# Performance work log

Hardware: AMD Instinct MI355X
Metric: run time of the kernel (lower is better)

## Reference

```python
import jax, jax.numpy as jnp
import numpy as np

# Dims from GlobalFractalRouterConfig defaults
B, D, FP, H, NF, A = 65536, 512, 64, 256, 4, 32


def _norm(x):
    # F.normalize(dim=-1) with eps=1e-12
    return x / jnp.clip(jnp.linalg.norm(x, axis=-1, keepdims=True), 1e-12)


def setup_inputs() -> dict:
    key = jax.random.key(0)
    ks = jax.random.split(key, 12)
    s = 0.02
    return {
        "features": jax.random.normal(ks[0], (B, D), jnp.float32),
        "source_fingerprint": jax.random.normal(ks[1], (FP,), jnp.float32),
        "target_fingerprint": jax.random.normal(ks[2], (FP,), jnp.float32),
        # field_generators: NF stacked (Linear(D+FP,H) -> GELU -> Linear(H,1))
        "Wf1": jax.random.normal(ks[3], (NF, D + FP, H), jnp.float32) * s,
        "bf1": jnp.zeros((NF, H), jnp.float32),
        "Wf2": jax.random.normal(ks[4], (NF, H), jnp.float32) * s,
        "bf2": jnp.zeros((NF,), jnp.float32),
        # compat_proj: Linear(2*FP, NF)
        "Wc": jax.random.normal(ks[5], (2 * FP, NF), jnp.float32) * s,
        "bc": jnp.zeros((NF,), jnp.float32),
        # gate_net: Linear(2*NF+FP, H) -> GELU -> Linear(H, D) -> Sigmoid
        "Wg1": jax.random.normal(ks[6], (2 * NF + FP, H), jnp.float32) * s,
        "bg1": jnp.zeros((H,), jnp.float32),
        "Wg2": jax.random.normal(ks[7], (H, D), jnp.float32) * s,
        "bg2": jnp.zeros((D,), jnp.float32),
        # AnchorBank
        "E": jax.random.normal(ks[8], (A, D), jnp.float32) * s,  # anchor_embeddings
        "Wfp": jax.random.normal(ks[9], (D, D), jnp.float32) * s,  # feature_proj
        "bfp": jnp.zeros((D,), jnp.float32),
        "Wfq": jax.random.normal(ks[10], (FP, D), jnp.float32) * s,  # fingerprint_proj
        "bfq": jnp.zeros((D,), jnp.float32),
    }


def _potential(feats, fp_vec, Wf1, bf1, Wf2, bf2):
    # AdjacentGate.compute_potential, all fields vectorized
    b = feats.shape[0]
    comb = jnp.concatenate(
        [feats, jnp.broadcast_to(fp_vec, (b, fp_vec.shape[0]))], axis=-1
    )  # [B, D+FP]
    h = jax.nn.gelu(jnp.einsum('bi,fih->bfh', comb, Wf1) + bf1, approximate=False)
    return jnp.einsum('bfh,fh->bf', h, Wf2) + bf2  # [B, NF]


def reference(features, source_fingerprint, target_fingerprint,
              Wf1, bf1, Wf2, bf2, Wc, bc, Wg1, bg1, Wg2, bg2,
              E, Wfp, bfp, Wfq, bfq):
    b = features.shape[0]
    # --- AdjacentGate ---
    p_src = _potential(features, source_fingerprint, Wf1, bf1, Wf2, bf2)
    p_tgt = _potential(features, target_fingerprint, Wf1, bf1, Wf2, bf2)
    gradient = p_tgt - p_src  # [B, NF]
    fp_comb = jnp.concatenate([source_fingerprint, target_fingerprint])  # [2*FP]
    compat = jnp.tanh(fp_comb @ Wc + bc)  # [NF]
    gate_in = jnp.concatenate(
        [gradient,
         jnp.broadcast_to(compat, (b, compat.shape[0])),
         jnp.broadcast_to(source_fingerprint, (b, source_fingerprint.shape[0]))],
        axis=-1)  # [B, 2*NF+FP]
    gate = jax.nn.sigmoid(
        jax.nn.gelu(gate_in @ Wg1 + bg1, approximate=False) @ Wg2 + bg2)  # [B, D]
    gated = features * gate
    # --- AnchorBank ---
    feat_proj = _norm(gated @ Wfp + bfp)  # [B, D]
    anchors_norm = _norm(E)  # [A, D]
    aff = feat_proj @ anchors_norm.T  # [B, A]
    fp_proj = source_fingerprint @ Wfq + bfq  # [D]
    aff = aff + 0.3 * (anchors_norm @ fp_proj)
    aff = jax.nn.softmax(aff, axis=-1)
    anchor_features = aff @ E  # [B, D]
    return gated + anchor_features
```

## Files before the change

### kernel.cpp

```cpp
#include <hip/hip_runtime.h>
#include <hip/hip_bf16.h>

typedef unsigned short u16;
typedef __attribute__((ext_vector_type(8))) __bf16 bf16x8;
typedef __attribute__((ext_vector_type(8))) short  s16x8;
typedef __attribute__((ext_vector_type(4))) short  s16x4;
typedef __attribute__((ext_vector_type(4))) float  f32x4;

#define NB 65536
#define OFF_GRAD   0u
#define OFF_SUMSQ  1048576u
#define OFF_CONSTS 1310720u
#define OFF_WF1T   1327104u
#define OFF_WG2T   2375680u
#define OFF_WFPT   2637824u
#define OFF_ET     3162112u
#define OFF_AFF    3194880u
#define OFF_GATED  7389184u
#define WS_NEEDED  74498048u
#define CI_SRC   0
#define CI_TGT   1024
#define CI_C0    2048
#define CI_INVE  2304
#define CI_ABIAS 2336

__device__ inline float bf2f(u16 u) { union { unsigned int i; float f; } v; v.i = ((unsigned int)u) << 16; return v.f; }
__device__ inline u16 f2bf(float f) { union { float f; unsigned int i; } v; v.f = f; return (u16)((v.i + 0x7fffu + ((v.i >> 16) & 1u)) >> 16); }
__device__ inline float gelu(float x) {
  float z = 1.5957691216f * x * (1.0f + 0.044715f * x * x);
  return x * __builtin_amdgcn_rcpf(1.0f + __expf(-z));
}
__device__ inline float sigm(float x) { return __builtin_amdgcn_rcpf(1.0f + __expf(-x)); }

typedef __attribute__((address_space(3))) unsigned int as3_u32;
typedef __attribute__((address_space(1))) unsigned int as1_u32;
__device__ __forceinline__ void gload16(const u16* g, u16* l) {
  __builtin_amdgcn_global_load_lds((const as1_u32*)g, (as3_u32*)l, 16, 0, 0);
}

__global__ __launch_bounds__(256) void k_cvt(const float* __restrict__ feat, u16* __restrict__ featbf) {
  int idx = (blockIdx.x << 8) + threadIdx.x;
  const float4* src = (const float4*)feat + (idx << 1);
  float4 v0 = src[0], v1 = src[1];
  s16x8 o;
  o[0] = (short)f2bf(v0.x); o[1] = (short)f2bf(v0.y);
  o[2] = (short)f2bf(v0.z); o[3] = (short)f2bf(v0.w);
  o[4] = (short)f2bf(v1.x); o[5] = (short)f2bf(v1.y);
  o[6] = (short)f2bf(v1.z); o[7] = (short)f2bf(v1.w);
  *(s16x8*)(featbf + (idx << 3)) = o;
}

__global__ __launch_bounds__(256) void k_pre(
    const float* __restrict__ sfp, const float* __restrict__ tfp,
    const float* __restrict__ wf1, const float* __restrict__ bf1,
    const float* __restrict__ wc,  const float* __restrict__ bc,
    const float* __restrict__ wg1, const float* __restrict__ bg1,
    const float* __restrict__ wfq, const float* __restrict__ bfq,
    const float* __restrict__ E,   float* __restrict__ consts)
{
  __shared__ float s_s[64], s_t[64], s_c[4], s_fp[512];
  const int t = threadIdx.x;
  const int b = blockIdx.x;
  if (t < 64) { s_s[t] = sfp[t]; s_t[t] = tfp[t]; }
  __syncthreads();
  if (b < 8) {
    if (t < 128) {
      int n = b * 128 + t;
      int f = n >> 8, h = n & 255;
      float as = bf1[f * 256 + h];
      float at = as;
      const float* col = wf1 + f * 147456 + 512 * 256 + h;
      #pragma unroll 8
// ... 37 lines not shown
  }
}

__global__ __launch_bounds__(256) void k_transpose(
    const float* __restrict__ wf1, const float* __restrict__ wg2,
    const float* __restrict__ wfp, const float* __restrict__ E,
    u16* __restrict__ ws16)
{
  int tile = blockIdx.x;
  const float* src; u16* dst; int K, N, tl;
  if (tile < 512)      { int f = tile >> 7; tl = tile & 127; src = wf1 + f * 147456; dst = ws16 + (OFF_WF1T >> 1) + f * 131072; K = 512; N = 256; }
  else if (tile < 640) { tl = tile - 512; src = wg2; dst = ws16 + (OFF_WG2T >> 1); K = 256; N = 512; }
  else if (tile < 896) { tl = tile - 640; src = wfp; dst = ws16 + (OFF_WFPT >> 1); K = 512; N = 512; }
  else                 { tl = tile - 896; src = E;   dst = ws16 + (OFF_ET   >> 1); K = 32;  N = 512; }
  int ntn = N >> 5;
  int r0 = (tl / ntn) << 5, c0 = (tl % ntn) << 5;
  __shared__ float T[32][33];
  const int t = threadIdx.x;
  {
    int r = t >> 3, c4 = (t & 7) << 2;
    float4 v = *(const float4*)(src + (r0 + r) * N + c0 + c4);
    T[r][c4] = v.x; T[r][c4 + 1] = v.y; T[r][c4 + 2] = v.z; T[r][c4 + 3] = v.w;
  }
  __syncthreads();
  {
    int c = t >> 3, r4 = (t & 7) << 2;
    s16x4 v;
    v[0] = (short)f2bf(T[r4 + 0][c]); v[1] = (short)f2bf(T[r4 + 1][c]);
    v[2] = (short)f2bf(T[r4 + 2][c]); v[3] = (short)f2bf(T[r4 + 3][c]);
    *(s16x4*)(dst + (c0 + c) * K + r0 + r4) = v;
  }
}

__global__ __launch_bounds__(256, 2) void k_potential(
    const u16* __restrict__ featbf, const u16* __restrict__ wf1t,
    const float* __restrict__ wf2,  const float* __restrict__ consts,
    float* __restrict__ grad)
{
  __shared__ u16 U[36864];
  const int wg = blockIdx.x;
  const int s  = ((wg & 7) << 8) + (wg >> 3);
  const int f  = s & 3;
  const int col0 = f << 8;
  const int row0 = (s >> 2) << 7;
  const int t = threadIdx.x;
  const int w = t >> 6, lane = t & 63, lr = lane & 15, lq = lane >> 4;
  const int gr  = lane >> 2;
  const int gcs = ((lane & 3) ^ ((lane >> 3) & 3)) << 3;
  const int ca  = (lq ^ ((lr >> 1) & 3)) << 3;

  f32x4 acc[2][16];
  #pragma unroll
  for (int i = 0; i < 2; ++i)
    #pragma unroll
    for (int j = 0; j < 16; ++j) { f32x4 z = {0.f, 0.f, 0.f, 0.f}; acc[i][j] = z; }

#define STAGE_P(bi, k0) { u16* bas = U + (bi) * 12288; \
    _Pragma("unroll") for (int j = 0; j < 2; ++j) { int rb = (j << 6) + (w << 4); \
      gload16(featbf + (row0 + rb + gr) * 512 + (k0) + gcs, bas + rb * 32); } \
    _Pragma("unroll") for (int j = 0; j < 4; ++j) { int rb = (j << 6) + (w << 4); \
      gload16(wf1t + (col0 + rb + gr) * 512 + (k0) + gcs, bas + 4096 + rb * 32); } }

#define COMP_P(bi) { const u16* bas = U + (bi) * 12288; bf16x8 a[2]; \
    _Pragma("unroll") for (int rt = 0; rt < 2; ++rt) \
      a[rt] = *(const bf16x8*)&bas[((w << 5) + (rt << 4) + lr) * 32 + ca]; \
    _Pragma("unroll") for (int ct = 0; ct < 16; ++ct) { \
      bf16x8 bb = *(const bf16x8*)&bas[4096 + ((ct << 4) + lr) * 32 + ca]; \
      acc[0][ct] = __builtin_amdgcn_mfma_f32_16x16x32_bf16(a[0], bb, acc[0][ct], 0, 0, 0); \
      acc[1][ct] = __builtin_amdgcn_mfma_f32_16x16x32_bf16(a[1], bb, acc[1][ct], 0, 0, 0); } }

  STAGE_P(0, 0);
  STAGE_P(1, 32);
  #pragma unroll
  for (int tt = 0; tt < 16; ++tt) {
    if (tt < 15) asm volatile("s_waitcnt vmcnt(6)\n\ts_barrier" ::: "memory");
    else         asm volatile("s_waitcnt vmcnt(0)\n\ts_barrier" ::: "memory");
    if (tt < 14) STAGE_P((tt + 2) % 3, (tt + 2) * 32);
    COMP_P(tt % 3);
  }
#undef STAGE_P
#undef COMP_P
  float part[2][4] = {{0, 0, 0, 0}, {0, 0, 0, 0}};
  #pragma unroll
  for (int ct = 0; ct < 16; ++ct) {
    int n = col0 + (ct << 4) + lr;
    float so = consts[CI_SRC + n];
    float to = consts[CI_TGT + n];
    float w2 = wf2[n];
    #pragma unroll
    for (int rt = 0; rt < 2; ++rt)
      #pragma unroll
      for (int j = 0; j < 4; ++j) {
        float c = acc[rt][ct][j];
        part[rt][j] += (gelu(c + to) - gelu(c + so)) * w2;
      }
  }
  #pragma unroll
  for (int m = 1; m <= 8; m <<= 1)
    #pragma unroll
    for (int rt = 0; rt < 2; ++rt)
      #pragma unroll
      for (int j = 0; j < 4; ++j)
        part[rt][j] += __shfl_xor(part[rt][j], m, 64);
  if (lr == 0) {
    #pragma unroll
    for (int rt = 0; rt < 2; ++rt)
      #pragma unroll
      for (int j = 0; j < 4; ++j) {
        int r = row0 + (w << 5) + (rt << 4) + (lq << 2) + j;
        grad[r * 4 + f] = part[rt][j];
      }
  }
}

__global__ __launch_bounds__(256, 2) void k_gate(
    const u16* __restrict__ featbf, const float* __restrict__ grad,
    const float* __restrict__ wg1,  const u16* __restrict__ wg2t,
    const float* __restrict__ bg2,  const float* __restrict__ consts,
    u16* __restrict__ gated)
{
  __shared__ u16 Hl[32768];
  __shared__ u16 Bl[2][128][32];
  const int wg = blockIdx.x;
  const int s  = ((wg & 7) << 8) + (wg >> 3);
  const int col0 = (s & 3) << 7;
  const int row0 = (s >> 2) << 7;
  const int t = threadIdx.x;
  const int w = t >> 6, lane = t & 63, lr = lane & 15, lq = lane >> 4;
  const int gr  = lane >> 2;
  const int gcs = ((lane & 3) ^ ((lane >> 3) & 3)) << 3;
  const int ca  = (lq ^ ((lr >> 1) & 3)) << 3;

#define STAGE_G(buf, k0) { \
    _Pragma("unroll") for (int j = 0; j < 2; ++j) { int rb = (j << 6) + (w << 4); \
      gload16(wg2t + (col0 + rb + gr) * 256 + (k0) + gcs, &Bl[buf][rb][0]); } }

  STAGE_G(0, 0);

  {
    float wv[4], c0v = consts[CI_C0 + t];
    const int tc = t >> 3, tw = t & 7;
    #pragma unroll
    for (int f = 0; f < 4; ++f) wv[f] = wg1[f * 256 + t];
    for (int i = 0; i < 128; ++i) {
// ... 28 lines not shown
    COMP_G(1, k0 + 32);
    __syncthreads();
  }
#undef STAGE_G
#undef COMP_G
  u16* Gl = Hl;
  #pragma unroll
  for (int ct = 0; ct < 8; ++ct) {
    int n = col0 + (ct << 4) + lr;
    float bv = bg2[n];
    #pragma unroll
    for (int rt = 0; rt < 2; ++rt)
      #pragma unroll
      for (int j = 0; j < 4; ++j) {
        int r = (w << 5) + (rt << 4) + (lq << 2) + j;
        Gl[r * 136 + (ct << 4) + lr] = f2bf(sigm(acc[rt][ct][j] + bv));
      }
  }
  __syncthreads();
  #pragma unroll
  for (int it = 0; it < 8; ++it) {
    int s2 = (it << 8) + t;
    int r = s2 >> 4, c8 = (s2 & 15) << 3;
    s16x8 f8 = *(const s16x8*)(featbf + (row0 + r) * 512 + col0 + c8);
    s16x8 g8 = *(const s16x8*)(Gl + r * 136 + c8);
    s16x8 o;
    #pragma unroll
    for (int j = 0; j < 8; ++j)
      o[j] = (short)f2bf(bf2f((u16)f8[j]) * bf2f((u16)g8[j]));
    *(s16x8*)(gated + (row0 + r) * 512 + col0 + c8) = o;
  }
}

__global__ __launch_bounds__(256, 2) void k_proj(
    const u16* __restrict__ gated, const u16* __restrict__ wfpt,
    const float* __restrict__ bfp, const float* __restrict__ E,
    float* __restrict__ aff32, float* __restrict__ sumsq)
{
  __shared__ u16 U[36864];
  const int wg = blockIdx.x;
  const int s  = ((wg & 7) << 7) + (wg >> 3);
  const int col0 = (s & 1) << 8;
  const int row0 = (s >> 1) << 7;
  const int t = threadIdx.x;
  const int w = t >> 6, lane = t & 63, lr = lane & 15, lq = lane >> 4;
  const int gr  = lane >> 2;
  const int gcs = ((lane & 3) ^ ((lane >> 3) & 3)) << 3;
  const int ca  = (lq ^ ((lr >> 1) & 3)) << 3;

  f32x4 acc[2][16];
  #pragma unroll
  for (int i = 0; i < 2; ++i)
    #pragma unroll
    for (int j = 0; j < 16; ++j) { f32x4 z = {0.f, 0.f, 0.f, 0.f}; acc[i][j] = z; }

#define STAGE_J(bi, k0) { u16* bas = U + (bi) * 12288; \
    _Pragma("unroll") for (int j = 0; j < 2; ++j) { int rb = (j << 6) + (w << 4); \
      gload16(gated + (row0 + rb + gr) * 512 + (k0) + gcs, bas + rb * 32); } \
    _Pragma("unroll") for (int j = 0; j < 4; ++j) { int rb = (j << 6) + (w << 4); \
      gload16(wfpt + (col0 + rb + gr) * 512 + (k0) + gcs, bas + 4096 + rb * 32); } }

#define COMP_J(bi) { const u16* bas = U + (bi) * 12288; bf16x8 a[2]; \
    _Pragma("unroll") for (int rt = 0; rt < 2; ++rt) \
      a[rt] = *(const bf16x8*)&bas[((w << 5) + (rt << 4) + lr) * 32 + ca]; \
    _Pragma("unroll") for (int ct = 0; ct < 16; ++ct) { \
      bf16x8 bb = *(const bf16x8*)&bas[4096 + ((ct << 4) + lr) * 32 + ca]; \
      acc[0][ct] = __builtin_amdgcn_mfma_f32_16x16x32_bf16(a[0], bb, acc[0][ct], 0, 0, 0); \
      acc[1][ct] = __builtin_amdgcn_mfma_f32_16x16x32_bf16(a[1], bb, acc[1][ct], 0, 0, 0); } }

  STAGE_J(0, 0);
  STAGE_J(1, 32);
  #pragma unroll
  for (int tt = 0; tt < 16; ++tt) {
    if (tt < 15) asm volatile("s_waitcnt vmcnt(6)\n\ts_barrier" ::: "memory");
    else         asm volatile("s_waitcnt vmcnt(0)\n\ts_barrier" ::: "memory");
    if (tt < 14) STAGE_J((tt + 2) % 3, (tt + 2) * 32);
    COMP_J(tt % 3);
  }
#undef STAGE_J
#undef COMP_J
  float part[2][4] = {{0, 0, 0, 0}, {0, 0, 0, 0}};
  #pragma unroll
  for (int ct = 0; ct < 16; ++ct) {
    float bv = bfp[col0 + (ct << 4) + lr];
    #pragma unroll
    for (int rt = 0; rt < 2; ++rt)
      #pragma unroll
      for (int j = 0; j < 4; ++j) {
        acc[rt][ct][j] += bv;
        part[rt][j] += acc[rt][ct][j] * acc[rt][ct][j];
      }
  }
  #pragma unroll
  for (int m = 1; m <= 8; m <<= 1)
    #pragma unroll
    for (int rt = 0; rt < 2; ++rt)
      #pragma unroll
      for (int j = 0; j < 4; ++j)
        part[rt][j] += __shfl_xor(part[rt][j], m, 64);
  if (lr == 0) {
    #pragma unroll
    for (int rt = 0; rt < 2; ++rt)
      #pragma unroll
      for (int j = 0; j < 4; ++j)
        atomicAdd(&sumsq[row0 + (w << 5) + (rt << 4) + (lq << 2) + j], part[rt][j]);
  }
  __syncthreads();
  {
    int a = t >> 3, cb = (t & 7) << 5;
    const float* ep = E + a * 512 + col0 + cb;
    u16* dp = U + 17408 + a * 264 + cb;
    #pragma unroll
    for (int i = 0; i < 8; ++i) {
      float4 v = *(const float4*)(ep + (i << 2));
      s16x4 b;
      b[0] = (short)f2bf(v.x); b[1] = (short)f2bf(v.y);
      b[2] = (short)f2bf(v.z); b[3] = (short)f2bf(v.w);
      *(s16x4*)(dp + (i << 2)) = b;
    }
  }
  f32x4 acc2[2][2];
  #pragma unroll
  for (int i = 0; i < 2; ++i)
    #pragma unroll
    for (int j = 0; j < 2; ++j) { f32x4 z = {0.f, 0.f, 0.f, 0.f}; acc2[i][j] = z; }
  #pragma unroll
  for (int half = 0; half < 2; ++half) {
    if (half) __syncthreads();
    #pragma unroll
    for (int ct = 0; ct < 8; ++ct)
      #pragma unroll
      for (int rt = 0; rt < 2; ++rt)
        #pragma unroll
        for (int j = 0; j < 4; ++j) {
          int r = (w << 5) + (rt << 4) + (lq << 2) + j;
          U[r * 136 + (ct << 4) + lr] = f2bf(acc[rt][(half << 3) + ct][j]);
        }
    __syncthreads();
    #pragma unroll
    for (int ks = 0; ks < 4; ++ks) {
      bf16x8 a0 = *(const bf16x8*)&U[((w << 5) + lr) * 136 + (ks << 5) + (lq << 3)];
      bf16x8 a1 = *(const bf16x8*)&U[((w << 5) + 16 + lr) * 136 + (ks << 5) + (lq << 3)];
      bf16x8 b0 = *(const bf16x8*)&U[17408 + lr * 264 + (half << 7) + (ks << 5) + (lq << 3)];
      bf16x8 b1 = *(const bf16x8*)&U[17408 + (16 + lr) * 264 + (half << 7) + (ks << 5) + (lq << 3)];
      acc2[0][0] = __builtin_amdgcn_mfma_f32_16x16x32_bf16(a0, b0, acc2[0][0], 0, 0, 0);
      acc2[0][1] = __builtin_amdgcn_mfma_f32_16x16x32_bf16(a0, b1, acc2[0][1], 0, 0, 0);
      acc2[1][0] = __builtin_amdgcn_mfma_f32_16x16x32_bf16(a1, b0, acc2[1][0], 0, 0, 0);
      acc2[1][1] = __builtin_amdgcn_mfma_f32_16x16x32_bf16(a1, b1, acc2[1][1], 0, 0, 0);
    }
  }
  #pragma unroll
  for (int rt = 0; rt < 2; ++rt)
    #pragma unroll
    for (int c2 = 0; c2 < 2; ++c2)
      #pragma unroll
      for (int j = 0; j < 4; ++j) {
        int r = row0 + (w << 5) + (rt << 4) + (lq << 2) + j;
        int a = (c2 << 4) + lr;
        atomicAdd(&aff32[(r << 5) + a], acc2[rt][c2][j]);
      }
}

__global__ __launch_bounds__(256) void k_softmax(
    const float* __restrict__ aff32, const float* __restrict__ sumsq,
    const float* __restrict__ consts, u16* __restrict__ aff)
{
  const int t = threadIdx.x;
  const int lane = t & 63, wv = t >> 6;
  const int a = lane & 31, rh = lane >> 5;
  float ive = consts[CI_INVE + a], ab = consts[CI_ABIAS + a];
  #pragma unroll
  for (int it = 0; it < 4; ++it) {
    int r = (blockIdx.x << 5) + (wv << 3) + (it << 1) + rh;
    float invy = 1.0f / fmaxf(sqrtf(sumsq[r]), 1e-12f);
    float v = aff32[(r << 5) + a] * ive * invy + ab;
    float mx = v;
    #pragma unroll
    for (int m = 1; m <= 16; m <<= 1) mx = fmaxf(mx, __shfl_xor(mx, m, 64));
    float e = __expf(v - mx);
    float sm = e;
    #pragma unroll
    for (int m = 1; m <= 16; m <<= 1) sm += __shfl_xor(sm, m, 64);
    aff[(r << 5) + a] = f2bf(e * (1.0f / sm));
  }
}

__global__ __launch_bounds__(256, 2) void k_out(
    const u16* __restrict__ gated, const u16* __restrict__ aff,
    const u16* __restrict__ et, float* __restrict__ out)
{
  __shared__ u16 ETl[512][40];
  __shared__ u16 Afl[64][40];
  __shared__ u16 Ol[64][520];
// ... 51 lines not shown
  const float* feat = (const float*)d_in[0];
  const float* sfp  = (const float*)d_in[1];
  const float* tfp  = (const float*)d_in[2];
  const float* wf1  = (const float*)d_in[3];
  const float* bf1  = (const float*)d_in[4];
  const float* wf2  = (const float*)d_in[5];
  const float* wc   = (const float*)d_in[7];
  const float* bc   = (const float*)d_in[8];
  const float* wg1  = (const float*)d_in[9];
  const float* bg1  = (const float*)d_in[10];
  const float* wg2  = (const float*)d_in[11];
  const float* bg2  = (const float*)d_in[12];
  const float* E    = (const float*)d_in[13];
  const float* wfp  = (const float*)d_in[14];
  const float* bfp  = (const float*)d_in[15];
  const float* wfq  = (const float*)d_in[16];
  const float* bfq  = (const float*)d_in[17];

  char* ws = (char*)d_ws;
  float* grad   = (float*)(ws + OFF_GRAD);
  float* sumsq  = (float*)(ws + OFF_SUMSQ);
  float* consts = (float*)(ws + OFF_CONSTS);
  u16* ws16  = (u16*)ws;
  u16* wf1t  = (u16*)(ws + OFF_WF1T);
  u16* wg2t  = (u16*)(ws + OFF_WG2T);
  u16* wfpt  = (u16*)(ws + OFF_WFPT);
  u16* et    = (u16*)(ws + OFF_ET);
  u16* aff   = (u16*)(ws + OFF_AFF);
  u16* gated = (u16*)(ws + OFF_GATED);
  float* aff32 = (float*)d_out;
  u16* featbf  = (u16*)d_out + 33554432;
  float* out = (float*)d_out;

  hipMemsetAsync(ws + OFF_SUMSQ, 0, 262144, stream);
  hipMemsetAsync(d_out, 0, 8388608, stream);
  k_cvt<<<dim3(16384), dim3(256), 0, stream>>>(feat, featbf);
  k_pre<<<dim3(10), dim3(256), 0, stream>>>(sfp, tfp, wf1, bf1, wc, bc, wg1, bg1, wfq, bfq, E, consts);
  k_transpose<<<dim3(912), dim3(256), 0, stream>>>(wf1, wg2, wfp, E, ws16);
  k_potential<<<dim3(2048), dim3(256), 0, stream>>>(featbf, wf1t, wf2, consts, grad);
  k_gate<<<dim3(2048), dim3(256), 0, stream>>>(featbf, grad, wg1, wg2t, bg2, consts, gated);
  k_proj<<<dim3(1024), dim3(256), 0, stream>>>(gated, wfpt, bfp, E, aff32, sumsq);
  k_softmax<<<dim3(2048), dim3(256), 0, stream>>>(aff32, sumsq, consts, aff);
  k_out<<<dim3(1024), dim3(256), 0, stream>>>(gated, aff, et, out);
}
```

Measured before the change: 608.2 us.

## Retile potential and proj GEMMs to 128x128 blocks with 2x2 warp layout

Both k_potential and k_proj drop their 128x256 per-block tiles, where each warp owned 32 rows by all columns, in favour of 128x128 tiles with a 2x2 arrangement of 64x64 warp tiles. They also replace the triple-buffered vmcnt pipeline with a simpler double buffer and raise occupancy to 3 blocks per CU. Because each block now covers only half a field's hidden columns, gradient partials go to grad through atomicAdd, so grad is zeroed by the widened memset. The intent is better register and LDS reuse per MFMA and more resident waves. The cost is twice as many blocks, more atomics, and a possibly weaker load pipeline.

```diff
diff --git a/kernel.cpp b/kernel.cpp
--- a/kernel.cpp
+++ b/kernel.cpp
@@ -141,63 +141,68 @@
   }
 }
 
-__global__ __launch_bounds__(256, 2) void k_potential(
+__global__ __launch_bounds__(256, 3) void k_potential(
     const u16* __restrict__ featbf, const u16* __restrict__ wf1t,
     const float* __restrict__ wf2,  const float* __restrict__ consts,
     float* __restrict__ grad)
 {
-  __shared__ u16 U[36864];
+  __shared__ u16 Al[2][128][32];
+  __shared__ u16 Bl[2][128][32];
   const int wg = blockIdx.x;
-  const int s  = ((wg & 7) << 8) + (wg >> 3);
-  const int f  = s & 3;
-  const int col0 = f << 8;
-  const int row0 = (s >> 2) << 7;
+  const int s  = ((wg & 7) << 9) + (wg >> 3);
+  const int col0 = (s & 7) << 7;
+  const int f    = col0 >> 8;
+  const int row0 = (s >> 3) << 7;
   const int t = threadIdx.x;
   const int w = t >> 6, lane = t & 63, lr = lane & 15, lq = lane >> 4;
   const int gr  = lane >> 2;
   const int gcs = ((lane & 3) ^ ((lane >> 3) & 3)) << 3;
   const int ca  = (lq ^ ((lr >> 1) & 3)) << 3;
-
-  f32x4 acc[2][16];
-  #pragma unroll
-  for (int i = 0; i < 2; ++i)
-    #pragma unroll
-    for (int j = 0; j < 16; ++j) { f32x4 z = {0.f, 0.f, 0.f, 0.f}; acc[i][j] = z; }
-
-#define STAGE_P(bi, k0) { u16* bas = U + (bi) * 12288; \
+  const int wr = (w >> 1) << 6;
+  const int wc = (w & 1) << 6;
+
+  f32x4 acc[4][4];
+  #pragma unroll
+  for (int i = 0; i < 4; ++i)
+    #pragma unroll
+    for (int j = 0; j < 4; ++j) { f32x4 z = {0.f, 0.f, 0.f, 0.f}; acc[i][j] = z; }
+
+#define STAGE_P(buf, k0) { \
     _Pragma("unroll") for (int j = 0; j < 2; ++j) { int rb = (j << 6) + (w << 4); \
-      gload16(featbf + (row0 + rb + gr) * 512 + (k0) + gcs, bas + rb * 32); } \
-    _Pragma("unroll") for (int j = 0; j < 4; ++j) { int rb = (j << 6) + (w << 4); \
-      gload16(wf1t + (col0 + rb + gr) * 512 + (k0) + gcs, bas + 4096 + rb * 32); } }
-
-#define COMP_P(bi) { const u16* bas = U + (bi) * 12288; bf16x8 a[2]; \
-    _Pragma("unroll") for (int rt = 0; rt < 2; ++rt) \
-      a[rt] = *(const bf16x8*)&bas[((w << 5) + (rt << 4) + lr) * 32 + ca]; \
-    _Pragma("unroll") for (int ct = 0; ct < 16; ++ct) { \
-      bf16x8 bb = *(const bf16x8*)&bas[4096 + ((ct << 4) + lr) * 32 + ca]; \
-      acc[0][ct] = __builtin_amdgcn_mfma_f32_16x16x32_bf16(a[0], bb, acc[0][ct], 0, 0, 0); \
-      acc[1][ct] = __builtin_amdgcn_mfma_f32_16x16x32_bf16(a[1], bb, acc[1][ct], 0, 0, 0); } }
+      gload16(featbf + (row0 + rb + gr) * 512 + (k0) + gcs, &Al[buf][rb][0]); \
+      gload16(wf1t   + (col0 + rb + gr) * 512 + (k0) + gcs, &Bl[buf][rb][0]); } }
+
+#define COMP_P(buf) { bf16x8 a[4], b[4]; \
+    _Pragma("unroll") for (int rt = 0; rt < 4; ++rt) \
+      a[rt] = *(const bf16x8*)&Al[buf][wr + (rt << 4) + lr][ca]; \
+    _Pragma("unroll") for (int ct = 0; ct < 4; ++ct) \
+      b[ct] = *(const bf16x8*)&Bl[buf][wc + (ct << 4) + lr][ca]; \
+    _Pragma("unroll") for (int rt = 0; rt < 4; ++rt) \
+      _Pragma("unroll") for (int ct = 0; ct < 4; ++ct) \
+        acc[rt][ct] = __builtin_amdgcn_mfma_f32_16x16x32_bf16(a[rt], b[ct], acc[rt][ct], 0, 0, 0); }
 
   STAGE_P(0, 0);
-  STAGE_P(1, 32);
-  #pragma unroll
-  for (int tt = 0; tt < 16; ++tt) {
-    if (tt < 15) asm volatile("s_waitcnt vmcnt(6)\n\ts_barrier" ::: "memory");
-    else         asm volatile("s_waitcnt vmcnt(0)\n\ts_barrier" ::: "memory");
-    if (tt < 14) STAGE_P((tt + 2) % 3, (tt + 2) * 32);
-    COMP_P(tt % 3);
+  __syncthreads();
+  #pragma unroll
+  for (int k0 = 0; k0 < 512; k0 += 64) {
+    STAGE_P(1, k0 + 32);
+    COMP_P(0);
+    __syncthreads();
+    if (k0 + 64 < 512) STAGE_P(0, k0 + 64);
+    COMP_P(1);
+    __syncthreads();
   }
 #undef STAGE_P
 #undef COMP_P
-  float part[2][4] = {{0, 0, 0, 0}, {0, 0, 0, 0}};
-  #pragma unroll
-  for (int ct = 0; ct < 16; ++ct) {
-    int n = col0 + (ct << 4) + lr;
+  float part[4][4] = {{0,0,0,0},{0,0,0,0},{0,0,0,0},{0,0,0,0}};
+  #pragma unroll
+  for (int ct = 0; ct < 4; ++ct) {
+    int n = col0 + wc + (ct << 4) + lr;
     float so = consts[CI_SRC + n];
     float to = consts[CI_TGT + n];
     float w2 = wf2[n];
     #pragma unroll
-    for (int rt = 0; rt < 2; ++rt)
+    for (int rt = 0; rt < 4; ++rt)
       #pragma unroll
       for (int j = 0; j < 4; ++j) {
         float c = acc[rt][ct][j];
@@ -207,17 +212,17 @@
   #pragma unroll
   for (int m = 1; m <= 8; m <<= 1)
     #pragma unroll
-    for (int rt = 0; rt < 2; ++rt)
+    for (int rt = 0; rt < 4; ++rt)
       #pragma unroll
       for (int j = 0; j < 4; ++j)
         part[rt][j] += __shfl_xor(part[rt][j], m, 64);
   if (lr == 0) {
     #pragma unroll
-    for (int rt = 0; rt < 2; ++rt)
+    for (int rt = 0; rt < 4; ++rt)
       #pragma unroll
       for (int j = 0; j < 4; ++j) {
-        int r = row0 + (w << 5) + (rt << 4) + (lq << 2) + j;
-        grad[r * 4 + f] = part[rt][j];
+        int r = row0 + wr + (rt << 4) + (lq << 2) + j;
+        atomicAdd(&grad[r * 4 + f], part[rt][j]);
       }
   }
 }
@@ -313,59 +318,64 @@
   }
 }
 
-__global__ __launch_bounds__(256, 2) void k_proj(
+__global__ __launch_bounds__(256, 3) void k_proj(
     const u16* __restrict__ gated, const u16* __restrict__ wfpt,
     const float* __restrict__ bfp, const float* __restrict__ E,
     float* __restrict__ aff32, float* __restrict__ sumsq)
 {
-  __shared__ u16 U[36864];
+  __shared__ u16 U[24576];
+  u16* A0 = U;  u16* B0 = U + 4096;  u16* A1 = U + 8192;  u16* B1 = U + 12288;
   const int wg = blockIdx.x;
-  const int s  = ((wg & 7) << 7) + (wg >> 3);
-  const int col0 = (s & 1) << 8;
-  const int row0 = (s >> 1) << 7;
+  const int s  = ((wg & 7) << 8) + (wg >> 3);
+  const int col0 = (s & 3) << 7;
+  const int row0 = (s >> 2) << 7;
   const int t = threadIdx.x;
   const int w = t >> 6, lane = t & 63, lr = lane & 15, lq = lane >> 4;
   const int gr  = lane >> 2;
   const int gcs = ((lane & 3) ^ ((lane >> 3) & 3)) << 3;
   const int ca  = (lq ^ ((lr >> 1) & 3)) << 3;
-
-  f32x4 acc[2][16];
-  #pragma unroll
-  for (int i = 0; i < 2; ++i)
-    #pragma unroll
-    for (int j = 0; j < 16; ++j) { f32x4 z = {0.f, 0.f, 0.f, 0.f}; acc[i][j] = z; }
-
-#define STAGE_J(bi, k0) { u16* bas = U + (bi) * 12288; \
+  const int wr = (w >> 1) << 6;
+  const int wc = (w & 1) << 6;
+
+  f32x4 acc[4][4];
+  #pragma unroll
+  for (int i = 0; i < 4; ++i)
+    #pragma unroll
+    for (int j = 0; j < 4; ++j) { f32x4 z = {0.f, 0.f, 0.f, 0.f}; acc[i][j] = z; }
+
+#define STAGE_J(Ab, Bb, k0) { \
     _Pragma("unroll") for (int j = 0; j < 2; ++j) { int rb = (j << 6) + (w << 4); \
-      gload16(gated + (row0 + rb + gr) * 512 + (k0) + gcs, bas + rb * 32); } \
-    _Pragma("unroll") for (int j = 0; j < 4; ++j) { int rb = (j << 6) + (w << 4); \
-      gload16(wfpt + (col0 + rb + gr) * 512 + (k0) + gcs, bas + 4096 + rb * 32); } }
-
-#define COMP_J(bi) { const u16* bas = U + (bi) * 12288; bf16x8 a[2]; \
-    _Pragma("unroll") for (int rt = 0; rt < 2; ++rt) \
-      a[rt] = *(const bf16x8*)&bas[((w << 5) + (rt << 4) + lr) * 32 + ca]; \
-    _Pragma("unroll") for (int ct = 0; ct < 16; ++ct) { \
-      bf16x8 bb = *(const bf16x8*)&bas[4096 + ((ct << 4) + lr) * 32 + ca]; \
-      acc[0][ct] = __builtin_amdgcn_mfma_f32_16x16x32_bf16(a[0], bb, acc[0][ct], 0, 0, 0); \
-      acc[1][ct] = __builtin_amdgcn_mfma_f32_16x16x32_bf16(a[1], bb, acc[1][ct], 0, 0, 0); } }
-
-  STAGE_J(0, 0);
-  STAGE_J(1, 32);
-  #pragma unroll
-  for (int tt = 0; tt < 16; ++tt) {
-    if (tt < 15) asm volatile("s_waitcnt vmcnt(6)\n\ts_barrier" ::: "memory");
-    else         asm volatile("s_waitcnt vmcnt(0)\n\ts_barrier" ::: "memory");
-    if (tt < 14) STAGE_J((tt + 2) % 3, (tt + 2) * 32);
-    COMP_J(tt % 3);
+      gload16(gated + (row0 + rb + gr) * 512 + (k0) + gcs, Ab + rb * 32); \
+      gload16(wfpt  + (col0 + rb + gr) * 512 + (k0) + gcs, Bb + rb * 32); } }
+
+#define COMP_J(Ab, Bb) { bf16x8 a[4], b[4]; \
+    _Pragma("unroll") for (int rt = 0; rt < 4; ++rt) \
+      a[rt] = *(const bf16x8*)&Ab[(wr + (rt << 4) + lr) * 32 + ca]; \
+    _Pragma("unroll") for (int ct = 0; ct < 4; ++ct) \
+      b[ct] = *(const bf16x8*)&Bb[(wc + (ct << 4) + lr) * 32 + ca]; \
+    _Pragma("unroll") for (int rt = 0; rt < 4; ++rt) \
+      _Pragma("unroll") for (int ct = 0; ct < 4; ++ct) \
+        acc[rt][ct] = __builtin_amdgcn_mfma_f32_16x16x32_bf16(a[rt], b[ct], acc[rt][ct], 0, 0, 0); }
+
+  STAGE_J(A0, B0, 0);
+  __syncthreads();
+  #pragma unroll
+  for (int k0 = 0; k0 < 512; k0 += 64) {
+    STAGE_J(A1, B1, k0 + 32);
+    COMP_J(A0, B0);
+    __syncthreads();
+    if (k0 + 64 < 512) STAGE_J(A0, B0, k0 + 64);
+    COMP_J(A1, B1);
+    __syncthreads();
   }
 #undef STAGE_J
 #undef COMP_J
-  float part[2][4] = {{0, 0, 0, 0}, {0, 0, 0, 0}};
-  #pragma unroll
-  for (int ct = 0; ct < 16; ++ct) {
-    float bv = bfp[col0 + (ct << 4) + lr];
-    #pragma unroll
-    for (int rt = 0; rt < 2; ++rt)
+  float part[4][4] = {{0,0,0,0},{0,0,0,0},{0,0,0,0},{0,0,0,0}};
+  #pragma unroll
+  for (int ct = 0; ct < 4; ++ct) {
+    float bv = bfp[col0 + wc + (ct << 4) + lr];
+    #pragma unroll
+    for (int rt = 0; rt < 4; ++rt)
       #pragma unroll
       for (int j = 0; j < 4; ++j) {
         acc[rt][ct][j] += bv;
@@ -375,24 +385,32 @@
   #pragma unroll
   for (int m = 1; m <= 8; m <<= 1)
     #pragma unroll
-    for (int rt = 0; rt < 2; ++rt)
+    for (int rt = 0; rt < 4; ++rt)
       #pragma unroll
       for (int j = 0; j < 4; ++j)
         part[rt][j] += __shfl_xor(part[rt][j], m, 64);
   if (lr == 0) {
     #pragma unroll
-    for (int rt = 0; rt < 2; ++rt)
+    for (int rt = 0; rt < 4; ++rt)
       #pragma unroll
       for (int j = 0; j < 4; ++j)
-        atomicAdd(&sumsq[row0 + (w << 5) + (rt << 4) + (lq << 2) + j], part[rt][j]);
-  }
-  __syncthreads();
+        atomicAdd(&sumsq[row0 + wr + (rt << 4) + (lq << 2) + j], part[rt][j]);
+  }
+  #pragma unroll
+  for (int rt = 0; rt < 4; ++rt)
+    #pragma unroll
+    for (int ct = 0; ct < 4; ++ct)
+      #pragma unroll
+      for (int j = 0; j < 4; ++j) {
+        int r = wr + (rt << 4) + (lq << 2) + j;
+        U[r * 136 + wc + (ct << 4) + lr] = f2bf(acc[rt][ct][j]);
+      }
   {
-    int a = t >> 3, cb = (t & 7) << 5;
-    const float* ep = E + a * 512 + col0 + cb;
-    u16* dp = U + 17408 + a * 264 + cb;
-    #pragma unroll
-    for (int i = 0; i < 8; ++i) {
+    int a = t >> 3, cb2 = (t & 7) << 4;
+    const float* ep = E + a * 512 + col0 + cb2;
+    u16* dp = U + 17408 + a * 136 + cb2;
+    #pragma unroll
+    for (int i = 0; i < 4; ++i) {
       float4 v = *(const float4*)(ep + (i << 2));
       s16x4 b;
       b[0] = (short)f2bf(v.x); b[1] = (short)f2bf(v.y);
@@ -400,35 +418,22 @@
       *(s16x4*)(dp + (i << 2)) = b;
     }
   }
+  __syncthreads();
   f32x4 acc2[2][2];
   #pragma unroll
   for (int i = 0; i < 2; ++i)
     #pragma unroll
     for (int j = 0; j < 2; ++j) { f32x4 z = {0.f, 0.f, 0.f, 0.f}; acc2[i][j] = z; }
   #pragma unroll
-  for (int half = 0; half < 2; ++half) {
-    if (half) __syncthreads();
-    #pragma unroll
-    for (int ct = 0; ct < 8; ++ct)
-      #pragma unroll
-      for (int rt = 0; rt < 2; ++rt)
-        #pragma unroll
-        for (int j = 0; j < 4; ++j) {
-          int r = (w << 5) + (rt << 4) + (lq << 2) + j;
-          U[r * 136 + (ct << 4) + lr] = f2bf(acc[rt][(half << 3) + ct][j]);
-        }
-    __syncthreads();
-    #pragma unroll
-    for (int ks = 0; ks < 4; ++ks) {
-      bf16x8 a0 = *(const bf16x8*)&U[((w << 5) + lr) * 136 + (ks << 5) + (lq << 3)];
-      bf16x8 a1 = *(const bf16x8*)&U[((w << 5) + 16 + lr) * 136 + (ks << 5) + (lq << 3)];
-      bf16x8 b0 = *(const bf16x8*)&U[17408 + lr * 264 + (half << 7) + (ks << 5) + (lq << 3)];
-      bf16x8 b1 = *(const bf16x8*)&U[17408 + (16 + lr) * 264 + (half << 7) + (ks << 5) + (lq << 3)];
-      acc2[0][0] = __builtin_amdgcn_mfma_f32_16x16x32_bf16(a0, b0, acc2[0][0], 0, 0, 0);
-      acc2[0][1] = __builtin_amdgcn_mfma_f32_16x16x32_bf16(a0, b1, acc2[0][1], 0, 0, 0);
-      acc2[1][0] = __builtin_amdgcn_mfma_f32_16x16x32_bf16(a1, b0, acc2[1][0], 0, 0, 0);
-      acc2[1][1] = __builtin_amdgcn_mfma_f32_16x16x32_bf16(a1, b1, acc2[1][1], 0, 0, 0);
-    }
+  for (int ks = 0; ks < 4; ++ks) {
+    bf16x8 a0 = *(const bf16x8*)&U[((w << 5) + lr) * 136 + (ks << 5) + (lq << 3)];
+    bf16x8 a1 = *(const bf16x8*)&U[((w << 5) + 16 + lr) * 136 + (ks << 5) + (lq << 3)];
+    bf16x8 b0 = *(const bf16x8*)&U[17408 + lr * 136 + (ks << 5) + (lq << 3)];
+    bf16x8 b1 = *(const bf16x8*)&U[17408 + (16 + lr) * 136 + (ks << 5) + (lq << 3)];
+    acc2[0][0] = __builtin_amdgcn_mfma_f32_16x16x32_bf16(a0, b0, acc2[0][0], 0, 0, 0);
+    acc2[0][1] = __builtin_amdgcn_mfma_f32_16x16x32_bf16(a0, b1, acc2[0][1], 0, 0, 0);
+    acc2[1][0] = __builtin_amdgcn_mfma_f32_16x16x32_bf16(a1, b0, acc2[1][0], 0, 0, 0);
+    acc2[1][1] = __builtin_amdgcn_mfma_f32_16x16x32_bf16(a1, b1, acc2[1][1], 0, 0, 0);
   }
   #pragma unroll
   for (int rt = 0; rt < 2; ++rt)
@@ -557,14 +562,14 @@
   u16* featbf  = (u16*)d_out + 33554432;
   float* out = (float*)d_out;
 
-  hipMemsetAsync(ws + OFF_SUMSQ, 0, 262144, stream);
+  hipMemsetAsync(ws + OFF_GRAD, 0, 1310720, stream);
   hipMemsetAsync(d_out, 0, 8388608, stream);
   k_cvt<<<dim3(16384), dim3(256), 0, stream>>>(feat, featbf);
   k_pre<<<dim3(10), dim3(256), 0, stream>>>(sfp, tfp, wf1, bf1, wc, bc, wg1, bg1, wfq, bfq, E, consts);
   k_transpose<<<dim3(912), dim3(256), 0, stream>>>(wf1, wg2, wfp, E, ws16);
-  k_potential<<<dim3(2048), dim3(256), 0, stream>>>(featbf, wf1t, wf2, consts, grad);
+  k_potential<<<dim3(4096), dim3(256), 0, stream>>>(featbf, wf1t, wf2, consts, grad);
   k_gate<<<dim3(2048), dim3(256), 0, stream>>>(featbf, grad, wg1, wg2t, bg2, consts, gated);
-  k_proj<<<dim3(1024), dim3(256), 0, stream>>>(gated, wfpt, bfp, E, aff32, sumsq);
+  k_proj<<<dim3(2048), dim3(256), 0, stream>>>(gated, wfpt, bfp, E, aff32, sumsq);
   k_softmax<<<dim3(2048), dim3(256), 0, stream>>>(aff32, sumsq, consts, aff);
   k_out<<<dim3(1024), dim3(256), 0, stream>>>(gated, aff, et, out);
 }
```

New measurement: 668.1 us. +9.8%, slower.

## Make potential and proj GEMMs persistent with weight slabs resident in LDS

Applied to the files above, without the earlier changes.

k_potential and k_proj become persistent kernels: 256 blocks of 512 threads, each keeping a full-K weight column slab in swizzled LDS for its whole run. Each block then streams 2048 rows of activations directly from global memory into registers, prefetching the next row tile. Because blocks now split output columns more finely, the gradient is accumulated with atomics and the grad region is zeroed up front. In k_proj the anchor-affinity GEMM is fused per row tile through a small per-wave LDS buffer, with E held in registers. This removes repeated weight staging and per-tile barriers, at the cost of more atomics and exposed global-load latency on the activation path.

```diff
diff --git a/kernel.cpp b/kernel.cpp
--- a/kernel.cpp
+++ b/kernel.cpp
@@ -38,6 +38,13 @@
   __builtin_amdgcn_global_load_lds((const as1_u32*)g, (as3_u32*)l, 16, 0, 0);
 }
 
+__device__ __forceinline__ bf16x8 pack8(const float* p) {
+  s16x8 sv;
+  #pragma unroll
+  for (int i = 0; i < 8; ++i) sv[i] = (short)f2bf(p[i]);
+  union { s16x8 s; bf16x8 b; } u; u.s = sv; return u.b;
+}
+
 __global__ __launch_bounds__(256) void k_cvt(const float* __restrict__ feat, u16* __restrict__ featbf) {
   int idx = (blockIdx.x << 8) + threadIdx.x;
   const float4* src = (const float4*)feat + (idx << 1);
@@ -141,84 +148,79 @@
   }
 }
 
-__global__ __launch_bounds__(256, 2) void k_potential(
+__global__ __launch_bounds__(512, 2) void k_potential(
     const u16* __restrict__ featbf, const u16* __restrict__ wf1t,
     const float* __restrict__ wf2,  const float* __restrict__ consts,
     float* __restrict__ grad)
 {
-  __shared__ u16 U[36864];
+  __shared__ u16 Bl[65536];
   const int wg = blockIdx.x;
-  const int s  = ((wg & 7) << 8) + (wg >> 3);
-  const int f  = s & 3;
-  const int col0 = f << 8;
-  const int row0 = (s >> 2) << 7;
-  const int t = threadIdx.x;
-  const int w = t >> 6, lane = t & 63, lr = lane & 15, lq = lane >> 4;
-  const int gr  = lane >> 2;
-  const int gcs = ((lane & 3) ^ ((lane >> 3) & 3)) << 3;
-  const int ca  = (lq ^ ((lr >> 1) & 3)) << 3;
-
-  f32x4 acc[2][16];
-  #pragma unroll
-  for (int i = 0; i < 2; ++i)
-    #pragma unroll
-    for (int j = 0; j < 16; ++j) { f32x4 z = {0.f, 0.f, 0.f, 0.f}; acc[i][j] = z; }
-
-#define STAGE_P(bi, k0) { u16* bas = U + (bi) * 12288; \
-    _Pragma("unroll") for (int j = 0; j < 2; ++j) { int rb = (j << 6) + (w << 4); \
-      gload16(featbf + (row0 + rb + gr) * 512 + (k0) + gcs, bas + rb * 32); } \
-    _Pragma("unroll") for (int j = 0; j < 4; ++j) { int rb = (j << 6) + (w << 4); \
-      gload16(wf1t + (col0 + rb + gr) * 512 + (k0) + gcs, bas + 4096 + rb * 32); } }
-
-#define COMP_P(bi) { const u16* bas = U + (bi) * 12288; bf16x8 a[2]; \
-    _Pragma("unroll") for (int rt = 0; rt < 2; ++rt) \
-      a[rt] = *(const bf16x8*)&bas[((w << 5) + (rt << 4) + lr) * 32 + ca]; \
-    _Pragma("unroll") for (int ct = 0; ct < 16; ++ct) { \
-      bf16x8 bb = *(const bf16x8*)&bas[4096 + ((ct << 4) + lr) * 32 + ca]; \
-      acc[0][ct] = __builtin_amdgcn_mfma_f32_16x16x32_bf16(a[0], bb, acc[0][ct], 0, 0, 0); \
-      acc[1][ct] = __builtin_amdgcn_mfma_f32_16x16x32_bf16(a[1], bb, acc[1][ct], 0, 0, 0); } }
-
-  STAGE_P(0, 0);
-  STAGE_P(1, 32);
-  #pragma unroll
-  for (int tt = 0; tt < 16; ++tt) {
-    if (tt < 15) asm volatile("s_waitcnt vmcnt(6)\n\ts_barrier" ::: "memory");
-    else         asm volatile("s_waitcnt vmcnt(0)\n\ts_barrier" ::: "memory");
-    if (tt < 14) STAGE_P((tt + 2) % 3, (tt + 2) * 32);
-    COMP_P(tt % 3);
-  }
-#undef STAGE_P
-#undef COMP_P
-  float part[2][4] = {{0, 0, 0, 0}, {0, 0, 0, 0}};
-  #pragma unroll
-  for (int ct = 0; ct < 16; ++ct) {
+  const int cb = wg & 7;
+  const int rg = wg >> 3;
+  const int col0 = cb << 7;
+  const int f = cb >> 1;
+  const int row0 = rg << 11;
+  const int t = threadIdx.x, w = t >> 6, lane = t & 63;
+  const int lr = lane & 15, lq = lane >> 4;
+  const int lsw = lr & 7;
+
+  #pragma unroll
+  for (int r = 0; r < 16; ++r) {
+    int col = (r << 3) + w;
+    gload16(wf1t + ((col0 + col) << 9) + ((lane ^ (col & 7)) << 3), Bl + (col << 9));
+  }
+  float so[8], to[8], w2[8];
+  #pragma unroll
+  for (int ct = 0; ct < 8; ++ct) {
     int n = col0 + (ct << 4) + lr;
-    float so = consts[CI_SRC + n];
-    float to = consts[CI_TGT + n];
-    float w2 = wf2[n];
-    #pragma unroll
-    for (int rt = 0; rt < 2; ++rt)
+    so[ct] = consts[CI_SRC + n]; to[ct] = consts[CI_TGT + n]; w2[ct] = wf2[n];
+  }
+  asm volatile("s_waitcnt vmcnt(0)" ::: "memory");
+  __syncthreads();
+
+  f32x4 acc[8];
+  #pragma unroll
+  for (int i = 0; i < 8; ++i) { f32x4 z = {0.f, 0.f, 0.f, 0.f}; acc[i] = z; }
+
+  const u16* pac = featbf + ((row0 + (w << 4) + lr) << 9) + (lq << 3);
+  bf16x8 ap[8];
+  #pragma unroll
+  for (int i = 0; i < 8; ++i) ap[i] = *(const bf16x8*)(pac + (i << 5));
+
+  for (int rt = 0; rt < 16; ++rt) {
+    const int rtn = (rt < 15) ? rt + 1 : rt;
+    const u16* pan = featbf + ((row0 + (rtn << 7) + (w << 4) + lr) << 9) + (lq << 3);
+    #pragma unroll
+    for (int ks = 0; ks < 16; ++ks) {
+      bf16x8 av = ap[ks & 7];
+      #pragma unroll
+      for (int ct = 0; ct < 8; ++ct) {
+        bf16x8 bb = *(const bf16x8*)&Bl[(((ct << 4) + lr) << 9) + (((((ks << 2) + lq)) ^ lsw) << 3)];
+        acc[ct] = __builtin_amdgcn_mfma_f32_16x16x32_bf16(av, bb, acc[ct], 0, 0, 0);
+      }
+      ap[ks & 7] = (ks < 8) ? *(const bf16x8*)(pac + ((ks + 8) << 5))
+                            : *(const bf16x8*)(pan + ((ks - 8) << 5));
+    }
+    pac = pan;
+    float part[4] = {0.f, 0.f, 0.f, 0.f};
+    #pragma unroll
+    for (int ct = 0; ct < 8; ++ct)
       #pragma unroll
       for (int j = 0; j < 4; ++j) {
-        float c = acc[rt][ct][j];
-        part[rt][j] += (gelu(c + to) - gelu(c + so)) * w2;
+        float c = acc[ct][j];
+        part[j] += (gelu(c + to[ct]) - gelu(c + so[ct])) * w2[ct];
+        acc[ct][j] = 0.f;
       }
-  }
-  #pragma unroll
-  for (int m = 1; m <= 8; m <<= 1)
-    #pragma unroll
-    for (int rt = 0; rt < 2; ++rt)
+    #pragma unroll
+    for (int m = 1; m <= 8; m <<= 1)
       #pragma unroll
       for (int j = 0; j < 4; ++j)
-        part[rt][j] += __shfl_xor(part[rt][j], m, 64);
-  if (lr == 0) {
-    #pragma unroll
-    for (int rt = 0; rt < 2; ++rt)
-      #pragma unroll
-      for (int j = 0; j < 4; ++j) {
-        int r = row0 + (w << 5) + (rt << 4) + (lq << 2) + j;
-        grad[r * 4 + f] = part[rt][j];
-      }
+        part[j] += __shfl_xor(part[j], m, 64);
+    if (lr == 0) {
+      #pragma unroll
+      for (int j = 0; j < 4; ++j)
+        atomicAdd(&grad[((row0 + (rt << 7) + (w << 4) + (lq << 2) + j) << 2) + f], part[j]);
+    }
   }
 }
 
@@ -313,133 +315,121 @@
   }
 }
 
-__global__ __launch_bounds__(256, 2) void k_proj(
+__global__ __launch_bounds__(512, 2) void k_proj(
     const u16* __restrict__ gated, const u16* __restrict__ wfpt,
     const float* __restrict__ bfp, const float* __restrict__ E,
     float* __restrict__ aff32, float* __restrict__ sumsq)
 {
-  __shared__ u16 U[36864];
+  __shared__ u16 Bl[32768];
+  __shared__ u16 Yb[8][2304];
   const int wg = blockIdx.x;
-  const int s  = ((wg & 7) << 7) + (wg >> 3);
-  const int col0 = (s & 1) << 8;
-  const int row0 = (s >> 1) << 7;
-  const int t = threadIdx.x;
-  const int w = t >> 6, lane = t & 63, lr = lane & 15, lq = lane >> 4;
-  const int gr  = lane >> 2;
-  const int gcs = ((lane & 3) ^ ((lane >> 3) & 3)) << 3;
-  const int ca  = (lq ^ ((lr >> 1) & 3)) << 3;
-
-  f32x4 acc[2][16];
+  const int cb = wg & 7;
+  const int rg = wg >> 3;
+  const int col0 = cb << 6;
+  const int row0 = rg << 11;
+  const int t = threadIdx.x, w = t >> 6, lane = t & 63;
+  const int lr = lane & 15, lq = lane >> 4;
+  const int lsw = lr & 7;
+
+  #pragma unroll
+  for (int r = 0; r < 8; ++r) {
+    int col = (r << 3) + w;
+    gload16(wfpt + ((col0 + col) << 9) + ((lane ^ (col & 7)) << 3), Bl + (col << 9));
+  }
+  float bv[4];
+  #pragma unroll
+  for (int ct = 0; ct < 4; ++ct) bv[ct] = bfp[col0 + (ct << 4) + lr];
+  bf16x8 Ef[2][2];
+  #pragma unroll
+  for (int c2 = 0; c2 < 2; ++c2)
+    #pragma unroll
+    for (int k2 = 0; k2 < 2; ++k2)
+      Ef[c2][k2] = pack8(E + (((c2 << 4) + lr) << 9) + col0 + (k2 << 5) + (lq << 3));
+  asm volatile("s_waitcnt vmcnt(0)" ::: "memory");
+  __syncthreads();
+
+  f32x4 acc[2][4];
   #pragma unroll
   for (int i = 0; i < 2; ++i)
     #pragma unroll
-    for (int j = 0; j < 16; ++j) { f32x4 z = {0.f, 0.f, 0.f, 0.f}; acc[i][j] = z; }
-
-#define STAGE_J(bi, k0) { u16* bas = U + (bi) * 12288; \
-    _Pragma("unroll") for (int j = 0; j < 2; ++j) { int rb = (j << 6) + (w << 4); \
-      gload16(gated + (row0 + rb + gr) * 512 + (k0) + gcs, bas + rb * 32); } \
-    _Pragma("unroll") for (int j = 0; j < 4; ++j) { int rb = (j << 6) + (w << 4); \
-      gload16(wfpt + (col0 + rb + gr) * 512 + (k0) + gcs, bas + 4096 + rb * 32); } }
-
-#define COMP_J(bi) { const u16* bas = U + (bi) * 12288; bf16x8 a[2]; \
-    _Pragma("unroll") for (int rt = 0; rt < 2; ++rt) \
-      a[rt] = *(const bf16x8*)&bas[((w << 5) + (rt << 4) + lr) * 32 + ca]; \
-    _Pragma("unroll") for (int ct = 0; ct < 16; ++ct) { \
-      bf16x8 bb = *(const bf16x8*)&bas[4096 + ((ct << 4) + lr) * 32 + ca]; \
-      acc[0][ct] = __builtin_amdgcn_mfma_f32_16x16x32_bf16(a[0], bb, acc[0][ct], 0, 0, 0); \
-      acc[1][ct] = __builtin_amdgcn_mfma_f32_16x16x32_bf16(a[1], bb, acc[1][ct], 0, 0, 0); } }
-
-  STAGE_J(0, 0);
-  STAGE_J(1, 32);
-  #pragma unroll
-  for (int tt = 0; tt < 16; ++tt) {
-    if (tt < 15) asm volatile("s_waitcnt vmcnt(6)\n\ts_barrier" ::: "memory");
-    else         asm volatile("s_waitcnt vmcnt(0)\n\ts_barrier" ::: "memory");
-    if (tt < 14) STAGE_J((tt + 2) % 3, (tt + 2) * 32);
-    COMP_J(tt % 3);
-  }
-#undef STAGE_J
-#undef COMP_J
-  float part[2][4] = {{0, 0, 0, 0}, {0, 0, 0, 0}};
-  #pragma unroll
-  for (int ct = 0; ct < 16; ++ct) {
-    float bv = bfp[col0 + (ct << 4) + lr];
-    #pragma unroll
-    for (int rt = 0; rt < 2; ++rt)
-      #pragma unroll
-      for (int j = 0; j < 4; ++j) {
-        acc[rt][ct][j] += bv;
-        part[rt][j] += acc[rt][ct][j] * acc[rt][ct][j];
+    for (int j = 0; j < 4; ++j) { f32x4 z = {0.f, 0.f, 0.f, 0.f}; acc[i][j] = z; }
+
+  const u16* pa0 = gated + ((row0 + (w << 5) + lr) << 9) + (lq << 3);
+  const u16* pa1 = pa0 + (16 << 9);
+  bf16x8 a0p[8], a1p[8];
+  #pragma unroll
+  for (int i = 0; i < 8; ++i) {
+    a0p[i] = *(const bf16x8*)(pa0 + (i << 5));
+    a1p[i] = *(const bf16x8*)(pa1 + (i << 5));
+  }
+
+  for (int rt = 0; rt < 8; ++rt) {
+    const int rtn = (rt < 7) ? rt + 1 : rt;
+    const u16* pn0 = gated + ((row0 + (rtn << 8) + (w << 5) + lr) << 9) + (lq << 3);
+    const u16* pn1 = pn0 + (16 << 9);
+    #pragma unroll
+    for (int ks = 0; ks < 16; ++ks) {
+      bf16x8 av0 = a0p[ks & 7], av1 = a1p[ks & 7];
+      #pragma unroll
+      for (int ct = 0; ct < 4; ++ct) {
+        bf16x8 bb = *(const bf16x8*)&Bl[(((ct << 4) + lr) << 9) + (((((ks << 2) + lq)) ^ lsw) << 3)];
+        acc[0][ct] = __builtin_amdgcn_mfma_f32_16x16x32_bf16(av0, bb, acc[0][ct], 0, 0, 0);
+        acc[1][ct] = __builtin_amdgcn_mfma_f32_16x16x32_bf16(av1, bb, acc[1][ct], 0, 0, 0);
       }
-  }
-  #pragma unroll
-  for (int m = 1; m <= 8; m <<= 1)
-    #pragma unroll
-    for (int rt = 0; rt < 2; ++rt)
-      #pragma unroll
-      for (int j = 0; j < 4; ++j)
-        part[rt][j] += __shfl_xor(part[rt][j], m, 64);
-  if (lr == 0) {
-    #pragma unroll
-    for (int rt = 0; rt < 2; ++rt)
-      #pragma unroll
-      for (int j = 0; j < 4; ++j)
-        atomicAdd(&sumsq[row0 + (w << 5) + (rt << 4) + (lq << 2) + j], part[rt][j]);
-  }
-  __syncthreads();
-  {
-    int a = t >> 3, cb = (t & 7) << 5;
-    const float* ep = E + a * 512 + col0 + cb;
-    u16* dp = U + 17408 + a * 264 + cb;
-    #pragma unroll
-    for (int i = 0; i < 8; ++i) {
-      float4 v = *(const float4*)(ep + (i << 2));
-      s16x4 b;
-      b[0] = (short)f2bf(v.x); b[1] = (short)f2bf(v.y);
-      b[2] = (short)f2bf(v.z); b[3] = (short)f2bf(v.w);
-      *(s16x4*)(dp + (i << 2)) = b;
-    }
-  }
-  f32x4 acc2[2][2];
-  #pragma unroll
-  for (int i = 0; i < 2; ++i)
-    #pragma unroll
-    for (int j = 0; j < 2; ++j) { f32x4 z = {0.f, 0.f, 0.f, 0.f}; acc2[i][j] = z; }
-  #pragma unroll
-  for (int half = 0; half < 2; ++half) {
-    if (half) __syncthreads();
-    #pragma unroll
-    for (int ct = 0; ct < 8; ++ct)
-      #pragma unroll
-      for (int rt = 0; rt < 2; ++rt)
+      a0p[ks & 7] = (ks < 8) ? *(const bf16x8*)(pa0 + ((ks + 8) << 5)) : *(const bf16x8*)(pn0 + ((ks - 8) << 5));
+      a1p[ks & 7] = (ks < 8) ? *(const bf16x8*)(pa1 + ((ks + 8) << 5)) : *(const bf16x8*)(pn1 + ((ks - 8) << 5));
+    }
+    pa0 = pn0; pa1 = pn1;
+    float part[2][4] = {{0, 0, 0, 0}, {0, 0, 0, 0}};
+    #pragma unroll
+    for (int h = 0; h < 2; ++h)
+      #pragma unroll
+      for (int ct = 0; ct < 4; ++ct)
         #pragma unroll
         for (int j = 0; j < 4; ++j) {
-          int r = (w << 5) + (rt << 4) + (lq << 2) + j;
-          U[r * 136 + (ct << 4) + lr] = f2bf(acc[rt][(half << 3) + ct][j]);
+          float y = acc[h][ct][j] + bv[ct];
+          part[h][j] += y * y;
+          Yb[w][((h << 4) + (lq << 2) + j) * 72 + (ct << 4) + lr] = f2bf(y);
+          acc[h][ct][j] = 0.f;
         }
-    __syncthreads();
-    #pragma unroll
-    for (int ks = 0; ks < 4; ++ks) {
-      bf16x8 a0 = *(const bf16x8*)&U[((w << 5) + lr) * 136 + (ks << 5) + (lq << 3)];
-      bf16x8 a1 = *(const bf16x8*)&U[((w << 5) + 16 + lr) * 136 + (ks << 5) + (lq << 3)];
-      bf16x8 b0 = *(const bf16x8*)&U[17408 + lr * 264 + (half << 7) + (ks << 5) + (lq << 3)];
-      bf16x8 b1 = *(const bf16x8*)&U[17408 + (16 + lr) * 264 + (half << 7) + (ks << 5) + (lq << 3)];
-      acc2[0][0] = __builtin_amdgcn_mfma_f32_16x16x32_bf16(a0, b0, acc2[0][0], 0, 0, 0);
-      acc2[0][1] = __builtin_amdgcn_mfma_f32_16x16x32_bf16(a0, b1, acc2[0][1], 0, 0, 0);
-      acc2[1][0] = __builtin_amdgcn_mfma_f32_16x16x32_bf16(a1, b0, acc2[1][0], 0, 0, 0);
-      acc2[1][1] = __builtin_amdgcn_mfma_f32_16x16x32_bf16(a1, b1, acc2[1][1], 0, 0, 0);
-    }
-  }
-  #pragma unroll
-  for (int rt = 0; rt < 2; ++rt)
-    #pragma unroll
-    for (int c2 = 0; c2 < 2; ++c2)
-      #pragma unroll
-      for (int j = 0; j < 4; ++j) {
-        int r = row0 + (w << 5) + (rt << 4) + (lq << 2) + j;
-        int a = (c2 << 4) + lr;
-        atomicAdd(&aff32[(r << 5) + a], acc2[rt][c2][j]);
-      }
+    #pragma unroll
+    for (int m = 1; m <= 8; m <<= 1)
+      #pragma unroll
+      for (int h = 0; h < 2; ++h)
+        #pragma unroll
+        for (int j = 0; j < 4; ++j)
+          part[h][j] += __shfl_xor(part[h][j], m, 64);
+    if (lr == 0) {
+      #pragma unroll
+      for (int h = 0; h < 2; ++h)
+        #pragma unroll
+        for (int j = 0; j < 4; ++j)
+          atomicAdd(&sumsq[row0 + (rt << 8) + (w << 5) + (h << 4) + (lq << 2) + j], part[h][j]);
+    }
+    f32x4 s2[2][2];
+    #pragma unroll
+    for (int i = 0; i < 2; ++i)
+      #pragma unroll
+      for (int j = 0; j < 2; ++j) { f32x4 z = {0.f, 0.f, 0.f, 0.f}; s2[i][j] = z; }
+    #pragma unroll
+    for (int k2 = 0; k2 < 2; ++k2) {
+      bf16x8 ay0 = *(const bf16x8*)&Yb[w][lr * 72 + (k2 << 5) + (lq << 3)];
+      bf16x8 ay1 = *(const bf16x8*)&Yb[w][(16 + lr) * 72 + (k2 << 5) + (lq << 3)];
+      s2[0][0] = __builtin_amdgcn_mfma_f32_16x16x32_bf16(ay0, Ef[0][k2], s2[0][0], 0, 0, 0);
+      s2[0][1] = __builtin_amdgcn_mfma_f32_16x16x32_bf16(ay0, Ef[1][k2], s2[0][1], 0, 0, 0);
+      s2[1][0] = __builtin_amdgcn_mfma_f32_16x16x32_bf16(ay1, Ef[0][k2], s2[1][0], 0, 0, 0);
+      s2[1][1] = __builtin_amdgcn_mfma_f32_16x16x32_bf16(ay1, Ef[1][k2], s2[1][1], 0, 0, 0);
+    }
+    #pragma unroll
+    for (int h = 0; h < 2; ++h)
+      #pragma unroll
+      for (int c2 = 0; c2 < 2; ++c2)
+        #pragma unroll
+        for (int j = 0; j < 4; ++j) {
+          int r = row0 + (rt << 8) + (w << 5) + (h << 4) + (lq << 2) + j;
+          atomicAdd(&aff32[(r << 5) + (c2 << 4) + lr], s2[h][c2][j]);
+        }
+  }
 }
 
 __global__ __launch_bounds__(256) void k_softmax(
@@ -557,14 +547,14 @@
   u16* featbf  = (u16*)d_out + 33554432;
   float* out = (float*)d_out;
 
-  hipMemsetAsync(ws + OFF_SUMSQ, 0, 262144, stream);
+  hipMemsetAsync(ws + OFF_GRAD, 0, 1310720, stream);
   hipMemsetAsync(d_out, 0, 8388608, stream);
   k_cvt<<<dim3(16384), dim3(256), 0, stream>>>(feat, featbf);
   k_pre<<<dim3(10), dim3(256), 0, stream>>>(sfp, tfp, wf1, bf1, wc, bc, wg1, bg1, wfq, bfq, E, consts);
   k_transpose<<<dim3(912), dim3(256), 0, stream>>>(wf1, wg2, wfp, E, ws16);
-  k_potential<<<dim3(2048), dim3(256), 0, stream>>>(featbf, wf1t, wf2, consts, grad);
+  k_potential<<<dim3(256), dim3(512), 0, stream>>>(featbf, wf1t, wf2, consts, grad);
   k_gate<<<dim3(2048), dim3(256), 0, stream>>>(featbf, grad, wg1, wg2t, bg2, consts, gated);
-  k_proj<<<dim3(1024), dim3(256), 0, stream>>>(gated, wfpt, bfp, E, aff32, sumsq);
+  k_proj<<<dim3(256), dim3(512), 0, stream>>>(gated, wfpt, bfp, E, aff32, sumsq);
   k_softmax<<<dim3(2048), dim3(256), 0, stream>>>(aff32, sumsq, consts, aff);
   k_out<<<dim3(1024), dim3(256), 0, stream>>>(gated, aff, et, out);
 }
```

After: 1.291 ms. +112.3%, slower.
